# Optimization experiments

Hardware: AMD Instinct MI355X
Metric: run time of the kernel (lower is better)

## Reference

```python
import jax, jax.numpy as jnp
import numpy as np

B, T, D, V, CD, NF = 2, 2048, 1024, 32000, 1024, 4
EPS_NORM = 1e-12
EPS_LN = 1e-5


def _gelu(x):
    return jax.nn.gelu(x, approximate=False)


def _l2norm(x):
    n = jnp.linalg.norm(x, axis=-1, keepdims=True)
    return x / jnp.maximum(n, EPS_NORM)


def setup_inputs() -> dict:
    key = jax.random.key(0)
    ks = jax.random.split(key, 24)
    s = 0.02
    inp = {
        "tokens": jax.random.randint(ks[0], (B, T), 0, V),
        "c_states": jax.random.normal(ks[1], (8, CD), dtype=jnp.float32),
        "embed": jax.random.normal(ks[2], (V, D), dtype=jnp.float32) * s,
        "pos_embed": jax.random.normal(ks[3], (T, D), dtype=jnp.float32) * s,
        # c_to_topo: Linear(c_dim,64) -> GELU -> Linear(64,2) -> Softplus (dead code in fwd, kept for completeness)
        "topo_W1": jax.random.normal(ks[4], (CD, 64), dtype=jnp.float32) * s,
        "topo_b1": jnp.zeros((64,), jnp.float32),
        "topo_W2": jax.random.normal(ks[5], (64, 2), dtype=jnp.float32) * s,
        "topo_b2": jnp.zeros((2,), jnp.float32),
        # c_to_thresh: Linear(c_dim,32) -> GELU -> Linear(32,NF) -> Sigmoid
        "thr_W1": jax.random.normal(ks[6], (CD, 32), dtype=jnp.float32) * s,
        "thr_b1": jnp.zeros((32,), jnp.float32),
        "thr_W2": jax.random.normal(ks[7], (32, NF), dtype=jnp.float32) * s,
        "thr_b2": jnp.zeros((NF,), jnp.float32),
        # simplex layers: NF x (Linear(2D,D) -> GELU -> Linear(D,D))
        "simp_W1": jax.random.normal(ks[8], (NF, 2 * D, D), dtype=jnp.float32) * s,
        "simp_b1": jnp.zeros((NF, D), jnp.float32),
        "simp_W2": jax.random.normal(ks[9], (NF, D, D), dtype=jnp.float32) * s,
        "simp_b2": jnp.zeros((NF, D), jnp.float32),
        # topo_integrate: Linear(D+2, 2D) -> GELU -> Linear(2D, D)
        "int_W1": jax.random.normal(ks[10], (D + 2, 2 * D), dtype=jnp.float32) * s,
        "int_b1": jnp.zeros((2 * D,), jnp.float32),
        "int_W2": jax.random.normal(ks[11], (2 * D, D), dtype=jnp.float32) * s,
        "int_b2": jnp.zeros((D,), jnp.float32),
        "ln_g": jnp.ones((D,), jnp.float32),
        "ln_b": jnp.zeros((D,), jnp.float32),
        "head_W": jax.random.normal(ks[12], (D, V), dtype=jnp.float32) * s,
    }
    return inp


def _forward(tokens, c_states, embed, pos_embed,
             topo_W1, topo_b1, topo_W2, topo_b2,
             thr_W1, thr_b1, thr_W2, thr_b2,
             simp_W1, simp_b1, simp_W2, simp_b2,
             int_W1, int_b1, int_W2, int_b2,
             ln_g, ln_b, head_W):
    b, t = tokens.shape
    x = embed[tokens] + pos_embed[jnp.arange(t)][None]          # [B,T,D]
    c_pooled = c_states.mean(axis=0)                            # [CD]
    thresholds = jax.nn.sigmoid(_gelu(c_pooled @ thr_W1 + thr_b1) @ thr_W2 + thr_b2)  # [NF]

    for level in range(NF):
        thresh = thresholds[level]
        x0 = x[0]                                               # [T,D] (module only uses batch elem 0)
        xn = _l2norm(x0)
        sim = xn @ xn.T                                         # [T,T]
        adj = jax.nn.sigmoid(10.0 * (sim - thresh))
        agg = adj @ x0                                          # dense message aggregation
        combined = jnp.concatenate([x0, agg], axis=-1)          # [T,2D]
        update = _gelu(combined @ simp_W1[level] + simp_b1[level]) @ simp_W2[level] + simp_b2[level]
        x = x + update[None] * 0.2                              # broadcast update across batch

    # approximate Betti numbers on detached embeddings
    xd = jax.lax.stop_gradient(x[0])
    xn = _l2norm(xd)
    sim = xn @ xn.T
    adj = jax.nn.sigmoid(10.0 * (sim - 0.5))
    degree = adj.sum(axis=-1)
    beta0 = (degree < 0.5).astype(jnp.float32).sum()
    n_edges = adj.sum() / 2.0
    beta1 = jax.nn.relu(n_edges - jnp.float32(t) + beta0 + 1.0)
    betti = jnp.stack([beta0, beta1])                           # [2]
    betti_exp = jnp.broadcast_to(betti[None, None, :], (b, t, 2))

    x = jnp.concatenate([x, betti_exp], axis=-1)                # [B,T,D+2]
    x = _gelu(x @ int_W1 + int_b1) @ int_W2 + int_b2            # [B,T,D]
    mu = x.mean(axis=-1, keepdims=True)
    var = x.var(axis=-1, keepdims=True)
    x = (x - mu) / jnp.sqrt(var + EPS_LN) * ln_g + ln_b
    return x @ head_W                                           # [B,T,V]


def reference(tokens, c_states, embed, pos_embed,
              topo_W1, topo_b1, topo_W2, topo_b2,
              thr_W1, thr_b1, thr_W2, thr_b2,
              simp_W1, simp_b1, simp_W2, simp_b2,
              int_W1, int_b1, int_W2, int_b2,
              ln_g, ln_b, head_W):
    return _forward(tokens, c_states, embed, pos_embed,
                    topo_W1, topo_b1, topo_W2, topo_b2,
                    thr_W1, thr_b1, thr_W2, thr_b2,
                    simp_W1, simp_b1, simp_W2, simp_b2,
                    int_W1, int_b1, int_W2, int_b2,
                    ln_g, ln_b, head_W)
```

## Files before the change

kernel.cpp:

```cpp
#include <hip/hip_runtime.h>

typedef __bf16 bf16;
using bf16x8 = __attribute__((ext_vector_type(8))) __bf16;
using bf16x4 = __attribute__((ext_vector_type(4))) __bf16;
using f32x4  = __attribute__((ext_vector_type(4))) float;

#define DEV __device__ __forceinline__

DEV float gelu_f(float x){ return 0.5f*x*(1.0f+erff(x*0.7071067811865475f)); }
DEV float sigm_f(float x){ return 1.0f/(1.0f+expf(-x)); }

DEV void gload16(const bf16* g, bf16* l){
    __builtin_amdgcn_global_load_lds(
        (const __attribute__((address_space(1))) void*)g,
        (__attribute__((address_space(3))) void*)l, 16, 0, 0);
}

enum { EPI_ADJ=0, EPI_BF16=1, EPI_GELU_BIAS=2, EPI_XUPD=3, EPI_BIAS_F32=4, EPI_F32=5 };

template<int BM,int BN,int WM,int WN,int EPI>
__global__ __launch_bounds__(WM*WN*64, 2)
void gemm_p(const bf16* __restrict__ A, const bf16* __restrict__ B,
            int M, int N, int K, void* __restrict__ Cout, int ldc,
            const float* __restrict__ bias, const float* __restrict__ scal, int sidx,
            float* __restrict__ xu0, float* __restrict__ xu1)
{
    constexpr int THREADS = WM*WN*64;
    constexpr int MR = BM/WM/16, NR = BN/WN/16;
    constexpr int ATILE = BM*64, BTILE = BN*64;
    constexpr int RR = THREADS/8;
    constexpr int VM = (BM+BN)/RR;
    __shared__ bf16 sm[2*(ATILE+BTILE)];

    const int nbm = M/BM, nbn = N/BN;
    const int nwg = nbm*nbn;
    int wg = blockIdx.x;
    wg = (wg&7)*(nwg>>3) + (wg>>3);
    const int by = wg % nbm, bx = wg / nbm;
    const int tid = threadIdx.x, lane = tid&63, wid = tid>>6;
    const int wm = wid / WN, wn = wid % WN;
    const int fr = lane&15, fq = lane>>4;

    const bf16* Ab = A + (long)(by*BM + (tid>>3))*K + (((tid&7) ^ ((tid>>3)&7))<<3);
    const bf16* Bb = B + (long)(bx*BN + (tid>>3))*K + (((tid&7) ^ ((tid>>3)&7))<<3);

    auto STAGE = [&](int tt, int cb){
        bf16* d = sm + cb*(ATILE+BTILE) + wid*512;
        const long ko = (long)tt*64;
#pragma unroll
        for (int g=0; g<BM/RR; ++g)
            gload16(Ab + (long)g*RR*K + ko, d + g*RR*64);
#pragma unroll
        for (int g=0; g<BN/RR; ++g)
            gload16(Bb + (long)g*RR*K + ko, d + ATILE + g*RR*64);
    };

    f32x4 acc[MR][NR] = {};
    const int nt = K >> 6;

    STAGE(0,0);
    STAGE(1,1);

    for (int t=0; t<nt; ++t){
        const bf16* bufA = sm + (t&1)*(ATILE+BTILE);
        const bf16* bufB = bufA + ATILE;
        if (t+1<nt){
            if constexpr (VM==6)      asm volatile("s_waitcnt vmcnt(6)" ::: "memory");
            else if constexpr (VM==8) asm volatile("s_waitcnt vmcnt(8)" ::: "memory");
            else                      asm volatile("s_waitcnt vmcnt(0)" ::: "memory");
        } else {
            asm volatile("s_waitcnt vmcnt(0)" ::: "memory");
        }
        __builtin_amdgcn_s_barrier();
        __builtin_amdgcn_sched_barrier(0);
#pragma unroll
        for (int ks=0; ks<2; ++ks){
            bf16x8 af[MR], bv[NR];
            const int ch = (((ks*4+fq) ^ (fr&7))<<3);
#pragma unroll
            for (int j=0;j<MR;++j)
                af[j] = *(const bf16x8*)&bufA[(wm*(MR*16) + j*16 + fr)*64 + ch];
#pragma unroll
            for (int j=0;j<NR;++j)
                bv[j] = *(const bf16x8*)&bufB[(wn*(NR*16) + j*16 + fr)*64 + ch];
            __builtin_amdgcn_s_setprio(1);
#pragma unroll
            for (int mi=0;mi<MR;++mi)
#pragma unroll
            for (int ni=0;ni<NR;++ni)
                acc[mi][ni] = __builtin_amdgcn_mfma_f32_16x16x32_bf16(
                    af[mi], bv[ni], acc[mi][ni], 0,0,0);
            __builtin_amdgcn_s_setprio(0);
        }
        asm volatile("s_waitcnt lgkmcnt(0)" ::: "memory");
        __builtin_amdgcn_s_barrier();
        if (t+2<nt) STAGE(t+2, t&1);
    }

    float thr = 0.f;
    if constexpr (EPI==EPI_ADJ) thr = scal[sidx];

#pragma unroll
    for (int mi=0;mi<MR;++mi){
#pragma unroll
        for (int ni=0;ni<NR;++ni){
            const int col = bx*BN + wn*(NR*16) + ni*16 + fr;
#pragma unroll
            for (int r=0;r<4;++r){
                const int row = by*BM + wm*(MR*16) + mi*16 + fq*4 + r;
                const float v = acc[mi][ni][r];
                const long ci = (long)row*ldc + col;
                if constexpr (EPI==EPI_ADJ)       ((bf16*)Cout)[ci] = (bf16)sigm_f(10.f*(v - thr));
                else if constexpr (EPI==EPI_BF16) ((bf16*)Cout)[ci] = (bf16)v;
                else if constexpr (EPI==EPI_GELU_BIAS) ((bf16*)Cout)[ci] = (bf16)gelu_f(v + bias[col]);
                else if constexpr (EPI==EPI_BIAS_F32)  ((float*)Cout)[ci] = v + bias[col];
                else if constexpr (EPI==EPI_F32)       ((float*)Cout)[ci] = v;
                else if constexpr (EPI==EPI_XUPD){
                    const float u = 0.2f*(v + bias[col]);
                    xu0[ci] += u;  xu1[ci] += u;
                }
            }
        }
    }
}

__global__ void prep_kernel(const float* __restrict__ cs,
                            const float* __restrict__ W1, const float* __restrict__ b1,
                            const float* __restrict__ W2, const float* __restrict__ b2,
                            float* __restrict__ thrs)
{
    __shared__ float cp[1024];
    __shared__ float part[8][32];
    __shared__ float h[32];
    const int tid = threadIdx.x;
    for (int j = tid; j < 1024; j += 256){
        float s = 0.f;
#pragma unroll
        for (int r = 0; r < 8; r++) s += cs[r*1024 + j];
        cp[j] = s * 0.125f;
    }
    __syncthreads();
    const int t = tid & 31, g = tid >> 5;
    float p = 0.f;
    for (int j = g*128; j < g*128+128; j++) p += cp[j] * W1[j*32 + t];
    part[g][t] = p;
    __syncthreads();
    if (tid < 32){
        float s = b1[tid];
#pragma unroll
        for (int q=0;q<8;q++) s += part[q][tid];
        h[tid] = gelu_f(s);
    }
    __syncthreads();
    if (tid < 4){
        float z = b2[tid];
        for (int k=0;k<32;k++) z += h[k]*W2[k*4 + tid];
        thrs[tid] = sigm_f(z);
    }
    if (tid == 4) thrs[4] = 0.5f;
}

__global__ void embed_kernel(const int* __restrict__ tok, const float* __restrict__ emb,
                             const float* __restrict__ pos, float* __restrict__ x)
{
    const long i = (long)blockIdx.x*256 + threadIdx.x;
    const int  d4 = i & 255;
    const long bt = i >> 8;
    const int  t  = (int)(bt & 2047);
    const int  token = tok[bt];
    f32x4 e = *(const f32x4*)(emb + (long)token*1024 + d4*4);
    f32x4 p = *(const f32x4*)(pos + (long)t*1024 + d4*4);
    *(f32x4*)(x + i*4) = e + p;
}

__global__ void transpose_f2b(const float* __restrict__ in, int ldin,
                              bf16* __restrict__ out, int ldout, int R, int C)
{
    __shared__ float tile[32][33];
    const int nbx = C >> 5;
    const int bx = blockIdx.x % nbx, by = blockIdx.x / nbx;
    const int tx = threadIdx.x & 31, ty = threadIdx.x >> 5;
#pragma unroll
    for (int i=0;i<32;i+=8)
        tile[ty+i][tx] = in[(long)(by*32+ty+i)*ldin + bx*32+tx];
    __syncthreads();
#pragma unroll
    for (int i=0;i<32;i+=8)
        out[(long)(bx*32+ty+i)*ldout + by*32+tx] = (bf16)tile[tx][ty+i];
}

__global__ void rownorm_kernel(const float* __restrict__ x, bf16* __restrict__ xn,
                               bf16* __restrict__ x0b, int ld0)
{
    const long t = blockIdx.x; const int tid = threadIdx.x;
    f32x4 v = *(const f32x4*)(x + t*1024 + tid*4);
    float s = v.x*v.x + v.y*v.y + v.z*v.z + v.w*v.w;
#pragma unroll
    for (int o=32;o>0;o>>=1) s += __shfl_down(s, o);
    __shared__ float red[4];
    if ((tid&63)==0) red[tid>>6] = s;
    __syncthreads();
    const float tot = red[0]+red[1]+red[2]+red[3];
    const float inv = 1.0f / fmaxf(sqrtf(tot), 1e-12f);
    bf16x4 a, b;
    a[0]=(bf16)(v.x*inv); a[1]=(bf16)(v.y*inv); a[2]=(bf16)(v.z*inv); a[3]=(bf16)(v.w*inv);
    b[0]=(bf16)v.x; b[1]=(bf16)v.y; b[2]=(bf16)v.z; b[3]=(bf16)v.w;
    *(bf16x4*)(xn  + t*1024 + tid*4) = a;
    *(bf16x4*)(x0b + t*ld0  + tid*4) = b;
}

__global__ void degree_kernel(const bf16* __restrict__ adj, float* __restrict__ deg)
{
    const long t = blockIdx.x; const int tid = threadIdx.x;
    bf16x8 v = *(const bf16x8*)(adj + t*2048 + tid*8);
    float s = 0.f;
#pragma unroll
    for (int j=0;j<8;j++) s += (float)v[j];
#pragma unroll
    for (int o=32;o>0;o>>=1) s += __shfl_down(s, o);
    __shared__ float red[4];
    if ((tid&63)==0) red[tid>>6] = s;
    __syncthreads();
    if (tid==0) deg[t] = red[0]+red[1]+red[2]+red[3];
}

__global__ void betti_kernel(const float* __restrict__ deg, float* __restrict__ betti)
{
    const int tid = threadIdx.x;
    float s = 0.f, c = 0.f;
#pragma unroll
    for (int i=0;i<8;i++){
        const float d = deg[tid*8 + i];
        s += d;  c += (d < 0.5f) ? 1.f : 0.f;
    }
#pragma unroll
    for (int o=32;o>0;o>>=1){ s += __shfl_down(s,o); c += __shfl_down(c,o); }
    __shared__ float ss[4], cc[4];
    if ((tid&63)==0){ ss[tid>>6]=s; cc[tid>>6]=c; }
    __syncthreads();
    if (tid==0){
        const float S = ss[0]+ss[1]+ss[2]+ss[3];
        const float C = cc[0]+cc[1]+cc[2]+cc[3];
        const float ne = 0.5f*S;
        const float b1 = ne - 2048.f + C + 1.f;
        betti[0] = C;
        betti[1] = b1 > 0.f ? b1 : 0.f;
    }
}

__global__ void b1eff_kernel(const float* __restrict__ ib1, const float* __restrict__ iW1,
                             const float* __restrict__ betti, float* __restrict__ out)
{
    const int j = blockIdx.x*256 + threadIdx.x;
    out[j] = ib1[j] + betti[0]*iW1[(long)1024*2048 + j] + betti[1]*iW1[(long)1025*2048 + j];
}

__global__ void f2b_kernel(const float* __restrict__ in, bf16* __restrict__ out)
{
    const long i = (long)blockIdx.x*256 + threadIdx.x;
    f32x4 a = *(const f32x4*)(in + i*8);
    f32x4 c = *(const f32x4*)(in + i*8 + 4);
    bf16x8 o;
    o[0]=(bf16)a.x; o[1]=(bf16)a.y; o[2]=(bf16)a.z; o[3]=(bf16)a.w;
    o[4]=(bf16)c.x; o[5]=(bf16)c.y; o[6]=(bf16)c.z; o[7]=(bf16)c.w;
    *(bf16x8*)(out + i*8) = o;
}

__global__ void ln_kernel(const float* __restrict__ y, const float* __restrict__ g,
                          const float* __restrict__ b, bf16* __restrict__ out)
{
    const long t = blockIdx.x; const int tid = threadIdx.x;
    f32x4 v = *(const f32x4*)(y + t*1024 + tid*4);
    float s  = v.x+v.y+v.z+v.w;
    float s2 = v.x*v.x+v.y*v.y+v.z*v.z+v.w*v.w;
#pragma unroll
    for (int o=32;o>0;o>>=1){ s += __shfl_down(s,o); s2 += __shfl_down(s2,o); }
    __shared__ float ss[4], qq[4];
    if ((tid&63)==0){ ss[tid>>6]=s; qq[tid>>6]=s2; }
    __syncthreads();
    const float S = ss[0]+ss[1]+ss[2]+ss[3], Q = qq[0]+qq[1]+qq[2]+qq[3];
    const float mu  = S * (1.f/1024.f);
    const float var = Q * (1.f/1024.f) - mu*mu;
    const float inv = rsqrtf(var + 1e-5f);
    f32x4 gv = *(const f32x4*)(g + tid*4);
    f32x4 bv = *(const f32x4*)(b + tid*4);
    bf16x4 o;
    o[0] = (bf16)((v.x - mu)*inv*gv.x + bv.x);
    o[1] = (bf16)((v.y - mu)*inv*gv.y + bv.y);
    o[2] = (bf16)((v.z - mu)*inv*gv.z + bv.z);
    o[3] = (bf16)((v.w - mu)*inv*gv.w + bv.w);
    *(bf16x4*)(out + t*1024 + tid*4) = o;
}

extern "C" void kernel_launch(void* const* d_in, const int* in_sizes, int n_in,
                              void* d_out, int out_size, void* d_ws, size_t ws_size,
                              hipStream_t stream)
{
    const int*   tokens = (const int*)  d_in[0];
    const float* cstate = (const float*)d_in[1];
    const float* embedW = (const float*)d_in[2];
    const float* posW   = (const float*)d_in[3];
    const float* thrW1  = (const float*)d_in[8];
    const float* thrb1  = (const float*)d_in[9];
    const float* thrW2  = (const float*)d_in[10];
    const float* thrb2  = (const float*)d_in[11];
    const float* simpW1 = (const float*)d_in[12];
    const float* simpb1 = (const float*)d_in[13];
    const float* simpW2 = (const float*)d_in[14];
    const float* simpb2 = (const float*)d_in[15];
    const float* intW1  = (const float*)d_in[16];
    const float* intb1  = (const float*)d_in[17];
    const float* intW2  = (const float*)d_in[18];
    const float* intb2  = (const float*)d_in[19];
    const float* lng    = (const float*)d_in[20];
    const float* lnb    = (const float*)d_in[21];
    const float* headW  = (const float*)d_in[22];
    float* out = (float*)d_out;

    size_t off = 0;
    auto carve = [&](size_t bytes) -> void* {
        void* p = (char*)d_ws + off;
        off += (bytes + 255) & ~(size_t)255;
        return p;
    };
    float* x_f32   = (float*)carve(16777216);
    bf16*  xn      = (bf16*) carve(4194304);
    bf16*  x0T     = (bf16*) carve(4194304);
    bf16*  comb    = (bf16*) carve(8388608);
    bf16*  adj     = (bf16*) carve(8388608);
    bf16*  h1      = (bf16*) carve(4194304);
    bf16*  xb      = (bf16*) carve(8388608);
    bf16*  w1T     = (bf16*) carve(16777216);
    bf16*  w2T     = (bf16*) carve(8388608);
    bf16*  i1T     = (bf16*) carve(4194304);
    bf16*  i2T     = (bf16*) carve(4194304);
    bf16*  hT      = (bf16*) carve(65536000);
    float* degree  = (float*)carve(8192);
    float* b1eff   = (float*)carve(8192);
    float* thrs    = (float*)carve(64);
    float* betti   = (float*)carve(64);
    bf16*  h2  = comb;
    float* yv  = x_f32;
    bf16*  xln = xn;

    const dim3 blk(256);
    const dim3 blk512(512);

    prep_kernel<<<1, blk, 0, stream>>>(cstate, thrW1, thrb1, thrW2, thrb2, thrs);
    embed_kernel<<<4096, blk, 0, stream>>>(tokens, embedW, posW, x_f32);

    for (int l=0;l<4;l++)
        transpose_f2b<<<(1024/32)*(2048/32), blk, 0, stream>>>(
            simpW1 + (long)l*2048*1024, 1024, w1T + (long)l*1024*2048, 2048, 2048, 1024);
    for (int l=0;l<4;l++)
        transpose_f2b<<<(1024/32)*(1024/32), blk, 0, stream>>>(
            simpW2 + (long)l*1024*1024, 1024, w2T + (long)l*1024*1024, 1024, 1024, 1024);
    transpose_f2b<<<(2048/32)*(1024/32), blk, 0, stream>>>(intW1, 2048, i1T, 1024, 1024, 2048);
    transpose_f2b<<<(1024/32)*(2048/32), blk, 0, stream>>>(intW2, 1024, i2T, 2048, 2048, 1024);
    transpose_f2b<<<(32000/32)*(1024/32), blk, 0, stream>>>(headW, 32000, hT, 1024, 1024, 32000);

    for (int l=0;l<4;l++){
        rownorm_kernel<<<2048, blk, 0, stream>>>(x_f32, xn, comb, 2048);
        transpose_f2b<<<(1024/32)*(2048/32), blk, 0, stream>>>(x_f32, 1024, x0T, 2048, 2048, 1024);
        gemm_p<128,128,2,2,EPI_ADJ><<<16*16, blk, 0, stream>>>(
            xn, xn, 2048, 2048, 1024, adj, 2048, nullptr, thrs, l, nullptr, nullptr);
        gemm_p<64,128,2,2,EPI_BF16><<<32*8, blk, 0, stream>>>(
            adj, x0T, 2048, 1024, 2048, comb + 1024, 2048, nullptr, nullptr, 0, nullptr, nullptr);
        gemm_p<64,128,2,2,EPI_GELU_BIAS><<<32*8, blk, 0, stream>>>(
            comb, w1T + (long)l*1024*2048, 2048, 1024, 2048, h1, 1024,
            simpb1 + l*1024, nullptr, 0, nullptr, nullptr);
        gemm_p<64,128,2,2,EPI_XUPD><<<32*8, blk, 0, stream>>>(
            h1, w2T + (long)l*1024*1024, 2048, 1024, 1024, nullptr, 1024,
            simpb2 + l*1024, nullptr, 0, x_f32, x_f32 + (long)2048*1024);
    }

    rownorm_kernel<<<2048, blk, 0, stream>>>(x_f32, xn, comb, 2048);
    gemm_p<128,128,2,2,EPI_ADJ><<<16*16, blk, 0, stream>>>(
        xn, xn, 2048, 2048, 1024, adj, 2048, nullptr, thrs, 4, nullptr, nullptr);
    degree_kernel<<<2048, blk, 0, stream>>>(adj, degree);
    betti_kernel<<<1, blk, 0, stream>>>(degree, betti);
    b1eff_kernel<<<8, blk, 0, stream>>>(intb1, intW1, betti, b1eff);

    f2b_kernel<<<2048, blk, 0, stream>>>(x_f32, xb);
    gemm_p<128,128,2,2,EPI_GELU_BIAS><<<32*16, blk, 0, stream>>>(
        xb, i1T, 4096, 2048, 1024, h2, 2048, b1eff, nullptr, 0, nullptr, nullptr);
    gemm_p<128,128,2,2,EPI_BIAS_F32><<<32*8, blk, 0, stream>>>(
        h2, i2T, 4096, 1024, 2048, yv, 1024, intb2, nullptr, 0, nullptr, nullptr);
    ln_kernel<<<4096, blk, 0, stream>>>(yv, lng, lnb, xln);
    gemm_p<256,256,2,4,EPI_F32><<<16*125, blk512, 0, stream>>>(
        xln, hT, 4096, 32000, 1024, out, 32000, nullptr, nullptr, 0, nullptr, nullptr);
}
```

Measured before the change: 900.3 us.

## Use BK=32 triple-buffered GEMM pipeline with single barrier per k-step

Shrinks the GEMM k-tile from 64 to 32 and moves from double to triple LDS buffering, so the next-next stage is issued right after a single barrier instead of after a second barrier. The swizzle is adjusted for 32-wide rows, and launch-bound occupancy hints are raised to 3-4 waves. The large vocab head GEMM switches from 256x256/512-thread tiles to 128x128/256-thread tiles. The aim is less synchronization and higher occupancy, at the cost of twice as many k-iterations and less data reuse in the head GEMM.

```diff
diff --git a/kernel.cpp b/kernel.cpp
--- a/kernel.cpp
+++ b/kernel.cpp
@@ -18,19 +18,21 @@
 
 enum { EPI_ADJ=0, EPI_BF16=1, EPI_GELU_BIAS=2, EPI_XUPD=3, EPI_BIAS_F32=4, EPI_F32=5 };
 
-template<int BM,int BN,int WM,int WN,int EPI>
-__global__ __launch_bounds__(WM*WN*64, 2)
+template<int BM,int BN,int WM,int WN,int MINW,int EPI>
+__global__ __launch_bounds__(WM*WN*64, MINW)
 void gemm_p(const bf16* __restrict__ A, const bf16* __restrict__ B,
             int M, int N, int K, void* __restrict__ Cout, int ldc,
             const float* __restrict__ bias, const float* __restrict__ scal, int sidx,
             float* __restrict__ xu0, float* __restrict__ xu1)
 {
+    constexpr int BK = 32;
     constexpr int THREADS = WM*WN*64;
     constexpr int MR = BM/WM/16, NR = BN/WN/16;
-    constexpr int ATILE = BM*64, BTILE = BN*64;
-    constexpr int RR = THREADS/8;
+    constexpr int ATILE = BM*BK, BTILE = BN*BK;
+    constexpr int CPR = BK/8;
+    constexpr int RR = THREADS/CPR;
     constexpr int VM = (BM+BN)/RR;
-    __shared__ bf16 sm[2*(ATILE+BTILE)];
+    __shared__ bf16 sm[3*(ATILE+BTILE)];
 
     const int nbm = M/BM, nbn = N/BN;
     const int nwg = nbm*nbn;
@@ -41,60 +43,59 @@
     const int wm = wid / WN, wn = wid % WN;
     const int fr = lane&15, fq = lane>>4;
 
-    const bf16* Ab = A + (long)(by*BM + (tid>>3))*K + (((tid&7) ^ ((tid>>3)&7))<<3);
-    const bf16* Bb = B + (long)(bx*BN + (tid>>3))*K + (((tid&7) ^ ((tid>>3)&7))<<3);
-
-    auto STAGE = [&](int tt, int cb){
-        bf16* d = sm + cb*(ATILE+BTILE) + wid*512;
-        const long ko = (long)tt*64;
+    const int srow = tid/CPR, skc = tid%CPR;
+    const int skey = (srow>>1)&3;
+    const bf16* Ab = A + (long)(by*BM + srow)*K + ((skc^skey)<<3);
+    const bf16* Bb = B + (long)(bx*BN + srow)*K + ((skc^skey)<<3);
+
+    auto STAGE = [&](int tt){
+        bf16* d = sm + (tt%3)*(ATILE+BTILE) + wid*512;
+        const long ko = (long)tt*BK;
 #pragma unroll
         for (int g=0; g<BM/RR; ++g)
-            gload16(Ab + (long)g*RR*K + ko, d + g*RR*64);
+            gload16(Ab + (long)g*RR*K + ko, d + g*RR*BK);
 #pragma unroll
         for (int g=0; g<BN/RR; ++g)
-            gload16(Bb + (long)g*RR*K + ko, d + ATILE + g*RR*64);
+            gload16(Bb + (long)g*RR*K + ko, d + ATILE + g*RR*BK);
     };
 
     f32x4 acc[MR][NR] = {};
-    const int nt = K >> 6;
-
-    STAGE(0,0);
-    STAGE(1,1);
+    const int nt = K >> 5;
+    const int key = (fr>>1)&3;
+    const int ch  = ((fq ^ key)<<3);
+
+    STAGE(0);
+    STAGE(1);
 
     for (int t=0; t<nt; ++t){
-        const bf16* bufA = sm + (t&1)*(ATILE+BTILE);
-        const bf16* bufB = bufA + ATILE;
         if (t+1<nt){
-            if constexpr (VM==6)      asm volatile("s_waitcnt vmcnt(6)" ::: "memory");
-            else if constexpr (VM==8) asm volatile("s_waitcnt vmcnt(8)" ::: "memory");
+            if constexpr (VM==3)      asm volatile("s_waitcnt vmcnt(3)" ::: "memory");
+            else if constexpr (VM==4) asm volatile("s_waitcnt vmcnt(4)" ::: "memory");
             else                      asm volatile("s_waitcnt vmcnt(0)" ::: "memory");
         } else {
             asm volatile("s_waitcnt vmcnt(0)" ::: "memory");
         }
         __builtin_amdgcn_s_barrier();
+        if (t+2<nt) STAGE(t+2);
+
+        const bf16* bufA = sm + (t%3)*(ATILE+BTILE);
+        const bf16* bufB = bufA + ATILE;
+        bf16x8 af[MR], bv[NR];
+#pragma unroll
+        for (int j=0;j<MR;++j)
+            af[j] = *(const bf16x8*)&bufA[(wm*(MR*16) + j*16 + fr)*BK + ch];
+#pragma unroll
+        for (int j=0;j<NR;++j)
+            bv[j] = *(const bf16x8*)&bufB[(wn*(NR*16) + j*16 + fr)*BK + ch];
+        __builtin_amdgcn_s_setprio(1);
+#pragma unroll
+        for (int mi=0;mi<MR;++mi)
+#pragma unroll
+        for (int ni=0;ni<NR;++ni)
+            acc[mi][ni] = __builtin_amdgcn_mfma_f32_16x16x32_bf16(
+                af[mi], bv[ni], acc[mi][ni], 0,0,0);
+        __builtin_amdgcn_s_setprio(0);
         __builtin_amdgcn_sched_barrier(0);
-#pragma unroll
-        for (int ks=0; ks<2; ++ks){
-            bf16x8 af[MR], bv[NR];
-            const int ch = (((ks*4+fq) ^ (fr&7))<<3);
-#pragma unroll
-            for (int j=0;j<MR;++j)
-                af[j] = *(const bf16x8*)&bufA[(wm*(MR*16) + j*16 + fr)*64 + ch];
-#pragma unroll
-            for (int j=0;j<NR;++j)
-                bv[j] = *(const bf16x8*)&bufB[(wn*(NR*16) + j*16 + fr)*64 + ch];
-            __builtin_amdgcn_s_setprio(1);
-#pragma unroll
-            for (int mi=0;mi<MR;++mi)
-#pragma unroll
-            for (int ni=0;ni<NR;++ni)
-                acc[mi][ni] = __builtin_amdgcn_mfma_f32_16x16x32_bf16(
-                    af[mi], bv[ni], acc[mi][ni], 0,0,0);
-            __builtin_amdgcn_s_setprio(0);
-        }
-        asm volatile("s_waitcnt lgkmcnt(0)" ::: "memory");
-        __builtin_amdgcn_s_barrier();
-        if (t+2<nt) STAGE(t+2, t&1);
     }
 
     float thr = 0.f;
@@ -344,7 +345,6 @@
     bf16*  xln = xn;
 
     const dim3 blk(256);
-    const dim3 blk512(512);
 
     prep_kernel<<<1, blk, 0, stream>>>(cstate, thrW1, thrb1, thrW2, thrb2, thrs);
     embed_kernel<<<4096, blk, 0, stream>>>(tokens, embedW, posW, x_f32);
@@ -362,31 +362,31 @@
     for (int l=0;l<4;l++){
         rownorm_kernel<<<2048, blk, 0, stream>>>(x_f32, xn, comb, 2048);
         transpose_f2b<<<(1024/32)*(2048/32), blk, 0, stream>>>(x_f32, 1024, x0T, 2048, 2048, 1024);
-        gemm_p<128,128,2,2,EPI_ADJ><<<16*16, blk, 0, stream>>>(
+        gemm_p<128,128,2,2,3,EPI_ADJ><<<16*16, blk, 0, stream>>>(
             xn, xn, 2048, 2048, 1024, adj, 2048, nullptr, thrs, l, nullptr, nullptr);
-        gemm_p<64,128,2,2,EPI_BF16><<<32*8, blk, 0, stream>>>(
+        gemm_p<64,128,2,2,4,EPI_BF16><<<32*8, blk, 0, stream>>>(
             adj, x0T, 2048, 1024, 2048, comb + 1024, 2048, nullptr, nullptr, 0, nullptr, nullptr);
-        gemm_p<64,128,2,2,EPI_GELU_BIAS><<<32*8, blk, 0, stream>>>(
+        gemm_p<64,128,2,2,4,EPI_GELU_BIAS><<<32*8, blk, 0, stream>>>(
             comb, w1T + (long)l*1024*2048, 2048, 1024, 2048, h1, 1024,
             simpb1 + l*1024, nullptr, 0, nullptr, nullptr);
-        gemm_p<64,128,2,2,EPI_XUPD><<<32*8, blk, 0, stream>>>(
+        gemm_p<64,128,2,2,4,EPI_XUPD><<<32*8, blk, 0, stream>>>(
             h1, w2T + (long)l*1024*1024, 2048, 1024, 1024, nullptr, 1024,
             simpb2 + l*1024, nullptr, 0, x_f32, x_f32 + (long)2048*1024);
     }
 
     rownorm_kernel<<<2048, blk, 0, stream>>>(x_f32, xn, comb, 2048);
-    gemm_p<128,128,2,2,EPI_ADJ><<<16*16, blk, 0, stream>>>(
+    gemm_p<128,128,2,2,3,EPI_ADJ><<<16*16, blk, 0, stream>>>(
         xn, xn, 2048, 2048, 1024, adj, 2048, nullptr, thrs, 4, nullptr, nullptr);
     degree_kernel<<<2048, blk, 0, stream>>>(adj, degree);
     betti_kernel<<<1, blk, 0, stream>>>(degree, betti);
     b1eff_kernel<<<8, blk, 0, stream>>>(intb1, intW1, betti, b1eff);
 
     f2b_kernel<<<2048, blk, 0, stream>>>(x_f32, xb);
-    gemm_p<128,128,2,2,EPI_GELU_BIAS><<<32*16, blk, 0, stream>>>(
+    gemm_p<128,128,2,2,3,EPI_GELU_BIAS><<<32*16, blk, 0, stream>>>(
         xb, i1T, 4096, 2048, 1024, h2, 2048, b1eff, nullptr, 0, nullptr, nullptr);
-    gemm_p<128,128,2,2,EPI_BIAS_F32><<<32*8, blk, 0, stream>>>(
+    gemm_p<128,128,2,2,3,EPI_BIAS_F32><<<32*8, blk, 0, stream>>>(
         h2, i2T, 4096, 1024, 2048, yv, 1024, intb2, nullptr, 0, nullptr, nullptr);
     ln_kernel<<<4096, blk, 0, stream>>>(yv, lng, lnb, xln);
-    gemm_p<256,256,2,4,EPI_F32><<<16*125, blk512, 0, stream>>>(
+    gemm_p<128,128,2,2,3,EPI_F32><<<32*250, blk, 0, stream>>>(
         xln, hT, 4096, 32000, 1024, out, 32000, nullptr, nullptr, 0, nullptr, nullptr);
 }
```

Result: slower. 1.067 ms (+18.5%).

## Add specialized 256x256 pipelined GEMM kernel for the vocab head projection

Applied to the files above, without the earlier changes.

Adds a dedicated bf16 MFMA GEMM kernel for the final 4096x32000x1024 head projection and launches it in place of the generic templated kernel. It loads tiles straight into LDS with async global-to-LDS loads, splitting each 64-wide K step into two 32-wide halves so that loads for later stages are issued while the current half is computed. It also remaps workgroup IDs in a strided pattern to improve cache locality, and raises wave priority around the MFMA block. The 128 KB LDS buffer limits residency to one workgroup per CU. The row layout in LDS may cause bank conflicts on fragment reads.

```diff
diff --git a/kernel.cpp b/kernel.cpp
--- a/kernel.cpp
+++ b/kernel.cpp
@@ -119,6 +119,95 @@
                     const float u = 0.2f*(v + bias[col]);
                     xu0[ci] += u;  xu1[ci] += u;
                 }
+            }
+        }
+    }
+}
+
+template<int EPI>
+__global__ __launch_bounds__(512, 2)
+void gemm8(const bf16* __restrict__ A, const bf16* __restrict__ B,
+           int M, int N, int K, void* __restrict__ Cout, int ldc,
+           const float* __restrict__ bias)
+{
+    __shared__ bf16 sm[65536];
+    const int nbm = M>>8, nbn = N>>8;
+    const int nwg = nbm*nbn;
+    int wg = blockIdx.x;
+    wg = (wg&7)*(nwg>>3) + (wg>>3);
+    const int by = wg % nbm, bx = wg / nbm;
+    const int tid = threadIdx.x, lane = tid&63, wid = tid>>6;
+    const int wm = wid>>2, wn = wid&3;
+    const int fr = lane&15, fq = lane>>4;
+
+    const int srow = tid>>2, sch = tid&3;
+    const bf16* Ag = A + (long)(by*256 + srow)*K + sch*8;
+    const bf16* Bg = B + (long)(bx*256 + srow)*K + sch*8;
+
+    auto STAGE = [&](int tt, int kh){
+        const int rg = ((tt&1)*2 + kh)*8192;
+        bf16* dA = sm + rg + wid*512;
+        bf16* dB = sm + 32768 + rg + wid*512;
+        const long ko = (long)tt*64 + kh*32;
+        gload16(Ag + ko,          dA);
+        gload16(Ag + 128*K + ko,  dA + 4096);
+        gload16(Bg + ko,          dB);
+        gload16(Bg + 128*K + ko,  dB + 4096);
+    };
+
+    f32x4 acc[8][4] = {};
+    const int nt = K >> 6;
+
+    STAGE(0,0); STAGE(0,1); STAGE(1,0);
+
+    for (int t=0; t<nt; ++t){
+#pragma unroll
+        for (int s=0; s<2; ++s){
+            if (t+1<nt)      asm volatile("s_waitcnt vmcnt(8)" ::: "memory");
+            else if (s==0)   asm volatile("s_waitcnt vmcnt(4)" ::: "memory");
+            else             asm volatile("s_waitcnt vmcnt(0)" ::: "memory");
+            __builtin_amdgcn_s_barrier();
+            __builtin_amdgcn_sched_barrier(0);
+            if (s==0){ if (t+1<nt) STAGE(t+1,1); }
+            else     { if (t+2<nt) STAGE(t+2,0); }
+            __builtin_amdgcn_sched_barrier(0);
+
+            const bf16* rA = sm + ((t&1)*2 + s)*8192;
+            const bf16* rB = rA + 32768;
+            bf16x8 af[8], bv[4];
+#pragma unroll
+            for (int j=0;j<8;++j)
+                af[j] = *(const bf16x8*)&rA[(wm*128 + j*16 + fr)*32 + fq*8];
+#pragma unroll
+            for (int j=0;j<4;++j)
+                bv[j] = *(const bf16x8*)&rB[(wn*64 + j*16 + fr)*32 + fq*8];
+            asm volatile("s_waitcnt lgkmcnt(0)" ::: "memory");
+            __builtin_amdgcn_sched_barrier(0);
+            __builtin_amdgcn_s_setprio(1);
+#pragma unroll
+            for (int mi=0;mi<8;++mi)
+#pragma unroll
+            for (int ni=0;ni<4;++ni)
+                acc[mi][ni] = __builtin_amdgcn_mfma_f32_16x16x32_bf16(
+                    af[mi], bv[ni], acc[mi][ni], 0,0,0);
+            __builtin_amdgcn_s_setprio(0);
+            __builtin_amdgcn_sched_barrier(0);
+        }
+    }
+
+#pragma unroll
+    for (int mi=0;mi<8;++mi){
+#pragma unroll
+        for (int ni=0;ni<4;++ni){
+            const int col = bx*256 + wn*64 + ni*16 + fr;
+#pragma unroll
+            for (int r=0;r<4;++r){
+                const int row = by*256 + wm*128 + mi*16 + fq*4 + r;
+                const float v = acc[mi][ni][r];
+                const long ci = (long)row*ldc + col;
+                if constexpr (EPI==EPI_F32)            ((float*)Cout)[ci] = v;
+                else if constexpr (EPI==EPI_BIAS_F32)  ((float*)Cout)[ci] = v + bias[col];
+                else                                   ((bf16*)Cout)[ci] = (bf16)v;
             }
         }
     }
@@ -387,6 +476,6 @@
     gemm_p<128,128,2,2,EPI_BIAS_F32><<<32*8, blk, 0, stream>>>(
         h2, i2T, 4096, 1024, 2048, yv, 1024, intb2, nullptr, 0, nullptr, nullptr);
     ln_kernel<<<4096, blk, 0, stream>>>(yv, lng, lnb, xln);
-    gemm_p<256,256,2,4,EPI_F32><<<16*125, blk512, 0, stream>>>(
-        xln, hT, 4096, 32000, 1024, out, 32000, nullptr, nullptr, 0, nullptr, nullptr);
-}
+    gemm8<EPI_F32><<<16*125, blk512, 0, stream>>>(
+        xln, hT, 4096, 32000, 1024, out, 32000, nullptr);
+}
```

Result: no change. 916.1 us (+1.7%).
